# Optimization experiments

Hardware: AMD Instinct MI355X
Metric: run time of the kernel (lower is better)

The kernel has to match this reference:

```python
import jax, jax.numpy as jnp
from jax import lax
import numpy as np

B, S, E, HID = 16, 7, 64, 64
RES = (64, 64); D = RES[0] * RES[1]
XLOW, XHIGH = -0.5, 0.5
RLOW, RHIGH = float(np.sqrt(0.01)), float(np.sqrt(0.05))
PIXEL_MULT = 1.0; N_ITER = 3; TSOFT = 1.0 / float(np.sqrt(E))

def _build_grid():
    ranges = [np.linspace(XLOW, XHIGH, r) for r in RES]
    g = np.stack(np.meshgrid(*ranges, indexing='xy'), axis=-1)
    g = g.reshape(RES[0], RES[1], -1).reshape(1, -1, 2)
    return jnp.asarray(g, dtype=jnp.float32)

ABS_GRID = _build_grid()  # [1, D, 2]

def _ln(x, g, b):
    m = jnp.mean(x, -1, keepdims=True)
    v = jnp.mean(jnp.square(x - m), -1, keepdims=True)
    return (x - m) * lax.rsqrt(v + 1e-5) * g + b

def _forward(data, slot_noise, pos_rand, conv0_w, conv0_b, conv1_w, conv1_b, conv2_w, conv2_b,
             dataN_g, dataN_b, queryN_g, queryN_b, toK_w, toK_b, toV_w, toV_b, dense_w, dense_b,
             mlp1_w, mlp1_b, mlp2_w, mlp2_b, gru_wih, gru_whh, gru_bih, gru_bhh,
             alpha1_w, alpha1_b, alpha2_w, alpha2_b, final1_w, final1_b, final2_w, final2_b,
             slots_mu, slots_logsigma):
    dn = ('NCHW', 'OIHW', 'NCHW')
    def conv(x, w, b):
        return lax.conv_general_dilated(x, w, (1, 1), 'SAME', dimension_numbers=dn) + b[None, :, None, None]
    # CNN encoder: Conv-ReLU x3, 'same' padding, k=5
    x = jax.nn.relu(conv(data, conv0_w, conv0_b))
    x = jax.nn.relu(conv(x, conv1_w, conv1_b))
    x = jax.nn.relu(conv(x, conv2_w, conv2_b))
    enc = x.transpose(0, 2, 3, 1).reshape(B, D, HID)
    enc = _ln(enc, dataN_g, dataN_b)

    queries = slots_mu + jnp.exp(slots_logsigma) * slot_noise  # [B,S,E]
    # init_slots: faithful replication (source indexes the SLOT dim, and swaps rlow/rhigh)
    pos_scale = pos_rand.at[:, :2, :].add(-0.5)
    pos_scale = pos_scale.at[:, -1, :].set((RLOW - RHIGH) * pos_rand[:, -1, :] + RHIGH)

    encK = enc @ toK_w + toK_b  # [B,D,E]
    encV = enc @ toV_w + toV_b

    def init_mlp(y):
        y = _ln(y, queryN_g, queryN_b)
        return jax.nn.relu(y @ mlp1_w + mlp1_b) @ mlp2_w + mlp2_b

    def get_kv(ps):
        # per-slot relative grid: [B,S,D,2]
        rel = (ABS_GRID[:, None] - ps[:, :, None, :2]) / ps[:, :, -1][:, :, None, None]
        eg = PIXEL_MULT * (rel @ dense_w + dense_b)  # [B,S,D,E]
        return init_mlp(encK[:, None] + eg), init_mlp(encV[:, None] + eg)

    def att_wts(q, k):
        logits = jnp.einsum('bse,bsde->bsd', q, k) * TSOFT
        att = jax.nn.softmax(logits, axis=1)  # softmax over slots
        wts = att / jnp.sum(att, -1, keepdims=True) + 1e-8
        return att, wts

    def update_frames(wts):
        new_pos = jnp.einsum('bsd,de->bse', wts, ABS_GRID[0])  # [B,S,2]
        d2 = jnp.sum(jnp.square(ABS_GRID[:, None] - new_pos[:, :, None]), -1)  # [B,S,D]
        new_scale = jnp.sqrt(jnp.einsum('bsd,bsd->bs', wts, d2))
        return jnp.concatenate([new_pos, new_scale[..., None]], -1)

    def gru(xg, h):
        gi = xg @ gru_wih.T + gru_bih
        gh = h @ gru_whh.T + gru_bhh
        ir, iz, inn = jnp.split(gi, 3, -1)
        hr, hz, hn = jnp.split(gh, 3, -1)
        r = jax.nn.sigmoid(ir + hr)
        z = jax.nn.sigmoid(iz + hz)
        n = jnp.tanh(inn + r * hn)
        return (1.0 - z) * n + z * h

    for _ in range(N_ITER):
        keys, vals = get_kv(pos_scale)
        att, wts = att_wts(_ln(queries, queryN_g, queryN_b), keys)
        pos_scale = update_frames(wts)
        upd = jnp.einsum('bsd,bsde->bse', wts, vals)
        queries = gru(upd.reshape(-1, E), queries.reshape(-1, E)).reshape(B, S, E)

    keys, _ = get_kv(pos_scale)
    att, wts = att_wts(_ln(queries, queryN_g, queryN_b), keys)
    nps = update_frames(wts)
    alpha = jax.nn.sigmoid(jax.nn.relu(queries @ alpha1_w + alpha1_b) @ alpha2_w + alpha2_b)
    slot_feat = jax.nn.relu(queries @ final1_w + final1_b) @ final2_w + final2_b + nps
    return queries, att, slot_feat, alpha

def setup_inputs() -> dict:
    ks = jax.random.split(jax.random.key(0), 20)
    f32 = jnp.float32
    def rn(i, shape, s):
        return jax.random.normal(ks[i], shape, f32) * s
    inp = dict(
        data=jax.random.normal(ks[0], (B, 1, RES[0], RES[1]), f32),
        slot_noise=jax.random.normal(ks[1], (B, S, E), f32),
        pos_rand=jax.random.uniform(ks[2], (B, S, 3), dtype=f32),
        conv0_w=rn(3, (HID, 1, 5, 5), 0.2), conv0_b=jnp.zeros(HID, f32),
        conv1_w=rn(4, (HID, HID, 5, 5), 0.025), conv1_b=jnp.zeros(HID, f32),
        conv2_w=rn(5, (HID, HID, 5, 5), 0.025), conv2_b=jnp.zeros(HID, f32),
        dataN_g=jnp.ones(HID, f32), dataN_b=jnp.zeros(HID, f32),
        queryN_g=jnp.ones(E, f32), queryN_b=jnp.zeros(E, f32),
        toK_w=rn(6, (HID, E), 0.125), toK_b=jnp.zeros(E, f32),
        toV_w=rn(7, (HID, E), 0.125), toV_b=jnp.zeros(E, f32),
        dense_w=rn(8, (2, E), 0.7), dense_b=jnp.zeros(E, f32),
        mlp1_w=rn(9, (E, E), 0.125), mlp1_b=jnp.zeros(E, f32),
        mlp2_w=rn(10, (E, E), 0.125), mlp2_b=jnp.zeros(E, f32),
        gru_wih=rn(11, (3 * E, E), 0.125), gru_whh=rn(12, (3 * E, E), 0.125),
        gru_bih=jnp.zeros(3 * E, f32), gru_bhh=jnp.zeros(3 * E, f32),
        alpha1_w=rn(13, (E, 32), 0.125), alpha1_b=jnp.zeros(32, f32),
        alpha2_w=rn(14, (32, 1), 0.18), alpha2_b=jnp.zeros(1, f32),
        final1_w=rn(15, (E, HID), 0.125), final1_b=jnp.zeros(HID, f32),
        final2_w=rn(16, (HID, 3), 0.125), final2_b=jnp.zeros(3, f32),
        slots_mu=rn(17, (1, 1, E), 1.0),
        slots_logsigma=rn(18, (1, 1, E), 0.01),
    )
    return inp

def reference(data, slot_noise, pos_rand, conv0_w, conv0_b, conv1_w, conv1_b, conv2_w, conv2_b,
              dataN_g, dataN_b, queryN_g, queryN_b, toK_w, toK_b, toV_w, toV_b, dense_w, dense_b,
              mlp1_w, mlp1_b, mlp2_w, mlp2_b, gru_wih, gru_whh, gru_bih, gru_bhh,
              alpha1_w, alpha1_b, alpha2_w, alpha2_b, final1_w, final1_b, final2_w, final2_b,
              slots_mu, slots_logsigma):
    return _forward(data, slot_noise, pos_rand, conv0_w, conv0_b, conv1_w, conv1_b, conv2_w, conv2_b,
                    dataN_g, dataN_b, queryN_g, queryN_b, toK_w, toK_b, toV_w, toV_b, dense_w, dense_b,
                    mlp1_w, mlp1_b, mlp2_w, mlp2_b, gru_wih, gru_whh, gru_bih, gru_bhh,
                    alpha1_w, alpha1_b, alpha2_w, alpha2_b, final1_w, final1_b, final2_w, final2_b,
                    slots_mu, slots_logsigma)
```

## Files before the change

### kernel.cpp

```cpp
#include <hip/hip_runtime.h>
#include <cmath>


#define RLOW_F 0.1f
#define RHIGH_F 0.22360679774997896f

typedef __attribute__((ext_vector_type(8))) __bf16 bf16x8;
typedef __attribute__((ext_vector_type(4))) float f32x4;

__device__ __forceinline__ float wsum64(float v){
  #pragma unroll
  for (int off = 32; off > 0; off >>= 1) v += __shfl_xor(v, off, 64);
  return v;
}
__device__ __forceinline__ float rdlane(float v, int l){
  return __int_as_float(__builtin_amdgcn_readlane(__float_as_int(v), l));
}
__device__ __forceinline__ unsigned short bf16bits(float v){
  __bf16 h = (__bf16)v;
  return *reinterpret_cast<unsigned short*>(&h);
}

__global__ void k_prep(const float* __restrict__ noise, const float* __restrict__ prand,
                       const float* __restrict__ mu, const float* __restrict__ logsig,
                       float* __restrict__ queries, float* __restrict__ ps){
  int row = blockIdx.x;
  int e = threadIdx.x;
  int s = row % 7;
  queries[row*64 + e] = mu[e] + expf(logsig[e]) * noise[row*64 + e];
  if (e < 3){
    float pr = prand[row*3 + e];
    float v;
    if (s < 2)      v = pr - 0.5f;
    else if (s == 6) v = (RLOW_F - RHIGH_F)*pr + RHIGH_F;
    else            v = pr;
    ps[row*3 + e] = v;
  }
}

__global__ __launch_bounds__(256) void k_conv0(const float* __restrict__ in,
                        const float* __restrict__ w, const float* __restrict__ bias,
                        unsigned short* __restrict__ out){
  int bi = blockIdx.x; int b = bi >> 6; int y = bi & 63;
  int t = threadIdx.x; int lane = t & 63; int xg = t >> 6;
  __shared__ float s_in[5*68];
  __shared__ float s_w[64*25];
  __shared__ float s_out[64*65];
  for (int i = t; i < 1600; i += 256) s_w[i] = w[i];
  for (int i = t; i < 340; i += 256){
    int r = i / 68, cx = i % 68;
    int yy = y + r - 2, gx = cx - 2;
    float v = 0.f;
    if (yy >= 0 && yy < 64 && gx >= 0 && gx < 64) v = in[(b*64 + yy)*64 + gx];
    s_in[r*68 + cx] = v;
  }
  __syncthreads();
  int o = lane;
  float bv = bias[o];
  float acc[16];
  #pragma unroll
  for (int k = 0; k < 16; k++) acc[k] = bv;
  #pragma unroll
  for (int ky = 0; ky < 5; ky++){
    float rv[20];
    const float4* p = reinterpret_cast<const float4*>(&s_in[ky*68 + xg*16]);
    #pragma unroll
    for (int q = 0; q < 5; q++){ float4 f = p[q]; rv[q*4]=f.x; rv[q*4+1]=f.y; rv[q*4+2]=f.z; rv[q*4+3]=f.w; }
    #pragma unroll
    for (int kx = 0; kx < 5; kx++){
      float wv = s_w[o*25 + ky*5 + kx];
      #pragma unroll
      for (int k = 0; k < 16; k++) acc[k] = fmaf(rv[k+kx], wv, acc[k]);
    }
  }
  #pragma unroll
  for (int k = 0; k < 16; k++) s_out[o*65 + xg*16 + k] = fmaxf(acc[k], 0.f);
  __syncthreads();
  for (int i = t; i < 4096; i += 256){
    int px = i >> 6, ch = i & 63;
    out[((size_t)(b*64 + y)*64 + px)*64 + ch] = bf16bits(s_out[ch*65 + px]);
  }
}

__global__ void k_packconv(const float* __restrict__ w, unsigned short* __restrict__ out){
  int idx = blockIdx.x*256 + threadIdx.x;
  if (idx >= 102400) return;
  int j = idx & 7;
  int l = (idx >> 3) & 63;
  int frag = idx >> 9;
  int nt = frag & 3;
  int ks = (frag >> 2) % 10;
  int dy = frag / 40;
  int q = l >> 4, cr = l & 15;
  int k = ks*32 + q*8 + j;
  int kx = k >> 6, ch = k & 63;
  int n = nt*16 + cr;
  out[idx] = bf16bits(w[((n*64 + ch)*5 + dy)*5 + kx]);
}

__global__ __launch_bounds__(256) void k_convm(const unsigned short* __restrict__ in_bf,
                        const unsigned short* __restrict__ wpack,
                        const float* __restrict__ bias,
                        const float* __restrict__ lng, const float* __restrict__ lnb,
                        unsigned short* __restrict__ out_bf, float* __restrict__ out_f,
                        int mode){
  int bi = blockIdx.x;
  int b = bi >> 4; int yg = bi & 15;
  int t = threadIdx.x; int wv = t >> 6; int l = t & 63;
  int q = l >> 4, cr = l & 15;
  int p0 = wv*16;

  __shared__ char lds[8*68*144];

  for (int ri = 0; ri < 8; ri++){
    int yy = yg*4 + ri - 2;
    bool rok = (yy >= 0 && yy < 64);
    const uint4* src = reinterpret_cast<const uint4*>(in_bf + (size_t)(b*64 + yy)*64*64);
    for (int i = t; i < 544; i += 256){
      int px = i >> 3, c8 = i & 7;
      uint4 v = {0u,0u,0u,0u};
      int gx = px - 2;
      if (rok && gx >= 0 && gx < 64) v = src[gx*8 + c8];
      *reinterpret_cast<uint4*>(&lds[ri*9792 + px*144 + c8*16]) = v;
    }
  }
  __syncthreads();

  f32x4 acc[4][4];
  #pragma unroll
  for (int r = 0; r < 4; r++)
    #pragma unroll
    for (int nt = 0; nt < 4; nt++) acc[r][nt] = (f32x4){0.f,0.f,0.f,0.f};

  const bf16x8* wp = reinterpret_cast<const bf16x8*>(wpack);
  for (int dy = 0; dy < 5; dy++){
    for (int ks = 0; ks < 10; ks++){
      bf16x8 Bf[4];
      int fbase = (dy*10 + ks)*4;
      #pragma unroll
      for (int nt = 0; nt < 4; nt++) Bf[nt] = wp[(fbase + nt)*64 + l];
      int aoff = (p0 + cr + (ks >> 1))*144 + (ks & 1)*64 + q*16;
      #pragma unroll
      for (int r = 0; r < 4; r++){
        bf16x8 a = *reinterpret_cast<const bf16x8*>(&lds[(r + dy)*9792 + aoff]);
        #pragma unroll
        for (int nt = 0; nt < 4; nt++)
          acc[r][nt] = __builtin_amdgcn_mfma_f32_16x16x32_bf16(a, Bf[nt], acc[r][nt], 0, 0, 0);
      }
    }
  }

  float bv[4];
  #pragma unroll
  for (int nt = 0; nt < 4; nt++) bv[nt] = bias[nt*16 + cr];

  if (mode == 0){
    #pragma unroll
    for (int r = 0; r < 4; r++){
      int y = yg*4 + r;
      #pragma unroll
      for (int reg = 0; reg < 4; reg++){
        int p = p0 + q*4 + reg;
        size_t base = ((size_t)(b*64 + y)*64 + p)*64;
        #pragma unroll
        for (int nt = 0; nt < 4; nt++)
          out_bf[base + nt*16 + cr] = bf16bits(fmaxf(acc[r][nt][reg] + bv[nt], 0.f));
      }
    }
  } else {
    float gv[4], bb[4];
    #pragma unroll
    for (int nt = 0; nt < 4; nt++){ gv[nt] = lng[nt*16 + cr]; bb[nt] = lnb[nt*16 + cr]; }
    #pragma unroll
    for (int r = 0; r < 4; r++){
      int y = yg*4 + r;
      #pragma unroll
      for (int reg = 0; reg < 4; reg++){
        int p = p0 + q*4 + reg;
        float v[4]; float s1 = 0.f, s2 = 0.f;
        #pragma unroll
        for (int nt = 0; nt < 4; nt++){
          v[nt] = fmaxf(acc[r][nt][reg] + bv[nt], 0.f);
          s1 += v[nt]; s2 += v[nt]*v[nt];
        }
        #pragma unroll
        for (int m = 1; m < 16; m <<= 1){ s1 += __shfl_xor(s1, m, 64); s2 += __shfl_xor(s2, m, 64); }
        float mean = s1 * (1.f/64.f);
        float var  = s2 * (1.f/64.f) - mean*mean;
        float rstd = 1.0f/sqrtf(var + 1e-5f);
        size_t base = ((size_t)b*4096 + y*64 + p)*64;
        #pragma unroll
        for (int nt = 0; nt < 4; nt++)
          out_f[base + nt*16 + cr] = (v[nt] - mean)*rstd*gv[nt] + bb[nt];
      }
    }
  }
}

__global__ void k_packw1(const float* __restrict__ w1, unsigned short* __restrict__ out){
  int idx = blockIdx.x*256 + threadIdx.x;
  int jj = idx & 7;
  int lane = (idx >> 3) & 63;
  int frag = idx >> 9;
  int ks = frag >> 2, nt = frag & 3;
  int q = lane >> 4, cr = lane & 15;
  int k = ks*32 + q*8 + jj;
  int n = nt*16 + cr;
  out[idx] = bf16bits(w1[k*64 + n]);
}

__global__ __launch_bounds__(256) void k_projm(const float* __restrict__ enc,
                       const unsigned short* __restrict__ kpack, const float* __restrict__ bk,
                       const unsigned short* __restrict__ vpack, const float* __restrict__ bvp,
                       float* __restrict__ K, float* __restrict__ V){
  int bi = blockIdx.x; int b = bi >> 6; int tile = bi & 63;
  int t = threadIdx.x; int wv = t >> 6; int l = t & 63;
  int q = l >> 4, cr = l & 15;
  int d0 = tile*64 + wv*16;

  const bf16x8* kp = reinterpret_cast<const bf16x8*>(kpack);
  const bf16x8* vp = reinterpret_cast<const bf16x8*>(vpack);
  bf16x8 KB[8], VB[8];
  #pragma unroll
  for (int f = 0; f < 8; f++){ KB[f] = kp[f*64 + l]; VB[f] = vp[f*64 + l]; }

  const float* er = enc + (size_t)(b*4096 + d0 + cr)*64;
  bf16x8 a0, a1;
  #pragma unroll
  for (int h = 0; h < 2; h++){
    const float4* e4 = reinterpret_cast<const float4*>(er + (h ? (32 + q*8) : (q*8)));
    #pragma unroll
    for (int p = 0; p < 2; p++){
      float4 e = e4[p];
      if (h == 0){ a0[p*4+0]=(__bf16)e.x; a0[p*4+1]=(__bf16)e.y; a0[p*4+2]=(__bf16)e.z; a0[p*4+3]=(__bf16)e.w; }
      else       { a1[p*4+0]=(__bf16)e.x; a1[p*4+1]=(__bf16)e.y; a1[p*4+2]=(__bf16)e.z; a1[p*4+3]=(__bf16)e.w; }
    }
  }

  f32x4 zero = {0.f,0.f,0.f,0.f};
  f32x4 aK[4], aV[4];
  #pragma unroll
  for (int nt = 0; nt < 4; nt++){
    aK[nt] = __builtin_amdgcn_mfma_f32_16x16x32_bf16(a0, KB[nt],     zero,   0, 0, 0);
    aK[nt] = __builtin_amdgcn_mfma_f32_16x16x32_bf16(a1, KB[4 + nt], aK[nt], 0, 0, 0);
    aV[nt] = __builtin_amdgcn_mfma_f32_16x16x32_bf16(a0, VB[nt],     zero,   0, 0, 0);
    aV[nt] = __builtin_amdgcn_mfma_f32_16x16x32_bf16(a1, VB[4 + nt], aV[nt], 0, 0, 0);
  }
  #pragma unroll
  for (int nt = 0; nt < 4; nt++){
    float bkv = bk[nt*16 + cr], bvv = bvp[nt*16 + cr];
    #pragma unroll
    for (int reg = 0; reg < 4; reg++){
      size_t base = ((size_t)b*4096 + d0 + q*4 + reg)*64 + nt*16 + cr;
      K[base] = aK[nt][reg] + bkv;
      V[base] = aV[nt][reg] + bvv;
    }
  }
}

__global__ void k_phaseprep(const float* __restrict__ queries, const float* __restrict__ ps,
                            const float* __restrict__ qg_, const float* __restrict__ qb_,
                            const float* __restrict__ dw, const float* __restrict__ db,
                            const float* __restrict__ mlp2w, const float* __restrict__ mlp2b,
                            float* __restrict__ absc, float* __restrict__ w2qc,
                            float* __restrict__ sum_att, float* __restrict__ upd){
  int row = blockIdx.x; int e = threadIdx.x;
  float q = queries[row*64 + e];
  float m = wsum64(q) * (1.f/64.f);
  float d = q - m;
  float var = wsum64(d*d) * (1.f/64.f);
  float qlnv = d * (1.0f/sqrtf(var + 1e-5f)) * qg_[e] + qb_[e];
  float px = ps[row*3], py = ps[row*3+1], sc = ps[row*3+2];
  float A  = dw[e]      / sc;
  float Bv = dw[64 + e] / sc;
  absc[(row*3+0)*64 + e] = A;
  absc[(row*3+1)*64 + e] = Bv;
  absc[(row*3+2)*64 + e] = db[e] - px*A - py*Bv;
  float acc = 0.f;
  const float* wrow = mlp2w + e*64;
  for (int j = 0; j < 64; j++) acc = fmaf(wrow[j], rdlane(qlnv, j), acc);
  w2qc[row*68 + e] = acc;
  float c2 = wsum64(mlp2b[e] * qlnv);
  if (e == 0) w2qc[row*68 + 64] = c2;
  upd[row*64 + e] = 0.f;
  if (e == 0) sum_att[row] = 0.f;
}

__global__ __launch_bounds__(256) void k_attn(const float* __restrict__ encX,
     const unsigned short* __restrict__ w1pack, const float* __restrict__ mlp1b,
     const float* __restrict__ absc, const float* __restrict__ qg_,
     const float* __restrict__ qb_, const float* __restrict__ w2qc,
     const float* __restrict__ att, const float* __restrict__ sum_att,
     float* __restrict__ outp, int mode){
  int t = threadIdx.x; int wv = t >> 6; int l = t & 63;
  int q = l >> 4, cr = l & 15;
  int bs = blockIdx.x >> 6; int tile = blockIdx.x & 63;
  int b = bs / 7;
  int m0 = tile*64 + wv*16;
  int drow = m0 + cr;

  const bf16x8* wp = reinterpret_cast<const bf16x8*>(w1pack);
  bf16x8 Bf[8];
  #pragma unroll
  for (int f = 0; f < 8; f++) Bf[f] = wp[f*64 + l];

  const float* Ac = absc + bs*192;
  const float* er = encX + (size_t)(b*4096 + drow)*64;
  float gx = -0.5f + (float)(drow & 63) * (1.f/63.f);
  float gy = -0.5f + (float)((drow >> 6) & 63) * (1.f/63.f);
  float x[16];
  #pragma unroll
  for (int h = 0; h < 2; h++){
    int fb = h ? (32 + q*8) : (q*8);
    const float4* e4 = reinterpret_cast<const float4*>(er + fb);
    const float4* A4 = reinterpret_cast<const float4*>(Ac + fb);
    const float4* B4 = reinterpret_cast<const float4*>(Ac + 64 + fb);
    const float4* C4 = reinterpret_cast<const float4*>(Ac + 128 + fb);
    #pragma unroll
    for (int p = 0; p < 2; p++){
      float4 e = e4[p], Av = A4[p], Bv = B4[p], Cv = C4[p];
      int o = h*8 + p*4;
      x[o+0] = e.x + gx*Av.x + gy*Bv.x + Cv.x;
      x[o+1] = e.y + gx*Av.y + gy*Bv.y + Cv.y;
      x[o+2] = e.z + gx*Av.z + gy*Bv.z + Cv.z;
      x[o+3] = e.w + gx*Av.w + gy*Bv.w + Cv.w;
    }
  }
  float s = 0.f;
  #pragma unroll
  for (int k = 0; k < 16; k++) s += x[k];
  s += __shfl_xor(s, 16, 64); s += __shfl_xor(s, 32, 64);
  float m = s * (1.f/64.f);
  float v = 0.f;
  #pragma unroll
  for (int k = 0; k < 16; k++){ float dd = x[k] - m; v += dd*dd; }
  v += __shfl_xor(v, 16, 64); v += __shfl_xor(v, 32, 64);
  float rstd = 1.0f/sqrtf(v * (1.f/64.f) + 1e-5f);

  bf16x8 a0, a1;
  #pragma unroll
  for (int h = 0; h < 2; h++){
    int fb = h ? (32 + q*8) : (q*8);
    const float4* g4 = reinterpret_cast<const float4*>(qg_ + fb);
    const float4* b4 = reinterpret_cast<const float4*>(qb_ + fb);
    #pragma unroll
    for (int p = 0; p < 2; p++){
      float4 gg = g4[p], bb = b4[p];
      int o = h*8 + p*4;
      float r0 = (x[o+0]-m)*rstd*gg.x + bb.x;
      float r1 = (x[o+1]-m)*rstd*gg.y + bb.y;
      float r2 = (x[o+2]-m)*rstd*gg.z + bb.z;
      float r3 = (x[o+3]-m)*rstd*gg.w + bb.w;
      if (h == 0){ a0[p*4+0]=(__bf16)r0; a0[p*4+1]=(__bf16)r1; a0[p*4+2]=(__bf16)r2; a0[p*4+3]=(__bf16)r3; }
      else       { a1[p*4+0]=(__bf16)r0; a1[p*4+1]=(__bf16)r1; a1[p*4+2]=(__bf16)r2; a1[p*4+3]=(__bf16)r3; }
    }
  }

  f32x4 zero = {0.f, 0.f, 0.f, 0.f};
  f32x4 acc[4];
  #pragma unroll
  for (int nt = 0; nt < 4; nt++){
    acc[nt] = __builtin_amdgcn_mfma_f32_16x16x32_bf16(a0, Bf[nt],     zero,    0, 0, 0);
    acc[nt] = __builtin_amdgcn_mfma_f32_16x16x32_bf16(a1, Bf[4 + nt], acc[nt], 0, 0, 0);
  }

  if (mode == 0){
    const float* wq = w2qc + bs*68;
    float c2 = wq[64];
    float p[4] = {0.f, 0.f, 0.f, 0.f};
    #pragma unroll
    for (int nt = 0; nt < 4; nt++){
      float bb  = mlp1b[nt*16 + cr];
      float wqv = wq[nt*16 + cr];
      #pragma unroll
      for (int reg = 0; reg < 4; reg++){
        float y = fmaxf(acc[nt][reg] + bb, 0.f);
        p[reg] = fmaf(y, wqv, p[reg]);
      }
    }
    #pragma unroll
    for (int reg = 0; reg < 4; reg++){
      #pragma unroll
      for (int off = 1; off < 16; off <<= 1) p[reg] += __shfl_xor(p[reg], off, 64);
    }
    if (cr == 0){
      #pragma unroll
      for (int reg = 0; reg < 4; reg++)
        outp[bs*4096 + m0 + q*4 + reg] = (p[reg] + c2) * 0.125f;
    }
  } else {
    float sa = sum_att[bs];
    float wr[4];
    #pragma unroll
    for (int reg = 0; reg < 4; reg++)
      wr[reg] = att[bs*4096 + m0 + q*4 + reg] / sa + 1e-8f;
    float pc[4] = {0.f, 0.f, 0.f, 0.f};
    #pragma unroll
    for (int nt = 0; nt < 4; nt++){
      float bb = mlp1b[nt*16 + cr];
      #pragma unroll
      for (int reg = 0; reg < 4; reg++)
        pc[nt] = fmaf(wr[reg], fmaxf(acc[nt][reg] + bb, 0.f), pc[nt]);
    }
    #pragma unroll
    for (int nt = 0; nt < 4; nt++){
      pc[nt] += __shfl_xor(pc[nt], 16, 64);
      pc[nt] += __shfl_xor(pc[nt], 32, 64);
    }
    __shared__ float red[4][64];
    if (q == 0){
      #pragma unroll
      for (int nt = 0; nt < 4; nt++) red[wv][nt*16 + cr] = pc[nt];
    }
    __syncthreads();
    if (t < 64) atomicAdd(&outp[bs*64 + t], red[0][t] + red[1][t] + red[2][t] + red[3][t]);
  }
}

__global__ void k_softmax(float* __restrict__ att, float* __restrict__ sum_att){
  int bi = blockIdx.x;
  int b = bi >> 4;
  int t = threadIdx.x;
  int d = (bi & 15)*256 + t;
  int lane = t & 63; int w = t >> 6;
  __shared__ float red[4];
  float l[7];
  #pragma unroll
  for (int s = 0; s < 7; s++) l[s] = att[(b*7+s)*4096 + d];
  float m = l[0];
  #pragma unroll
  for (int s = 1; s < 7; s++) m = fmaxf(m, l[s]);
  float sum = 0.f;
  #pragma unroll
  for (int s = 0; s < 7; s++){ l[s] = expf(l[s] - m); sum += l[s]; }
  for (int s = 0; s < 7; s++){
    float a = l[s] / sum;
    att[(b*7+s)*4096 + d] = a;
    float ws = wsum64(a);
    if (lane == 0) red[w] = ws;
    __syncthreads();
    if (t == 0) atomicAdd(&sum_att[b*7+s], red[0]+red[1]+red[2]+red[3]);
    __syncthreads();
  }
}

__global__ void k_frames(const float* __restrict__ att, const float* __restrict__ sum_att,
                         float* __restrict__ psout, float* __restrict__ sumw){
  int bs = blockIdx.x; int t = threadIdx.x;
  float sa = sum_att[bs];
  float a0 = 0.f, ax = 0.f, ay = 0.f, a2 = 0.f;
  for (int d = t; d < 4096; d += 256){
    float wv = att[bs*4096 + d] / sa + 1e-8f;
    float gx = -0.5f + (float)(d & 63) * (1.f/63.f);
    float gy = -0.5f + (float)(d >> 6) * (1.f/63.f);
    a0 += wv; ax += wv*gx; ay += wv*gy; a2 += wv*(gx*gx + gy*gy);
  }
  __shared__ float red[4][4];
  int lane = t & 63, w = t >> 6;
  a0 = wsum64(a0); ax = wsum64(ax); ay = wsum64(ay); a2 = wsum64(a2);
  if (lane == 0){ red[w][0]=a0; red[w][1]=ax; red[w][2]=ay; red[w][3]=a2; }
  __syncthreads();
  if (t == 0){
    float W0=0,Wx=0,Wy=0,Wg=0;
    for (int k = 0; k < 4; k++){ W0+=red[k][0]; Wx+=red[k][1]; Wy+=red[k][2]; Wg+=red[k][3]; }
    float s2 = Wg - (Wx*Wx + Wy*Wy)*(2.f - W0);
    psout[bs*3+0] = Wx; psout[bs*3+1] = Wy; psout[bs*3+2] = sqrtf(fmaxf(s2, 0.f));
    sumw[bs] = W0;
  }
}

__global__ void k_gru(const float* __restrict__ upd, float* __restrict__ queries,
                      const float* __restrict__ wih, const float* __restrict__ whh,
                      const float* __restrict__ bih, const float* __restrict__ bhh,
                      const float* __restrict__ mlp2w, const float* __restrict__ mlp2b,
                      const float* __restrict__ sumw){
  int row = blockIdx.x; int t = threadIdx.x;
  __shared__ float us[64], hs[64], xs[64], gis[192], ghs[192];
  if (t < 64){ us[t] = upd[row*64 + t]; hs[t] = queries[row*64 + t]; }
  __syncthreads();
  if (t < 64){
    float a = sumw[row] * mlp2b[t];
    for (int i = 0; i < 64; i++) a = fmaf(us[i], mlp2w[i*64 + t], a);
    xs[t] = a;
  }
  __syncthreads();
  float gi = bih[t], gh = bhh[t];
  for (int e = 0; e < 64; e++){
    gi = fmaf(wih[t*64 + e], xs[e], gi);
    gh = fmaf(whh[t*64 + e], hs[e], gh);
  }
  gis[t] = gi; ghs[t] = gh;
  __syncthreads();
  if (t < 64){
    float r = 1.0f/(1.0f + expf(-(gis[t]      + ghs[t])));
    float z = 1.0f/(1.0f + expf(-(gis[64+t]   + ghs[64+t])));
    float n = tanhf(gis[128+t] + r*ghs[128+t]);
    queries[row*64 + t] = (1.0f - z)*n + z*hs[t];
  }
}

__global__ void k_final(const float* __restrict__ queries, const float* __restrict__ nps,
                        const float* __restrict__ a1w, const float* __restrict__ a1b,
                        const float* __restrict__ a2w, const float* __restrict__ a2b,
                        const float* __restrict__ f1w, const float* __restrict__ f1b,
                        const float* __restrict__ f2w, const float* __restrict__ f2b,
                        float* __restrict__ out){
  int bs = blockIdx.x; int e = threadIdx.x;
  __shared__ float qs[64], hf[64], ha[32];
  float q = queries[bs*64 + e];
  qs[e] = q;
  out[bs*64 + e] = q;
  __syncthreads();
  float accf = f1b[e];
  for (int i = 0; i < 64; i++) accf = fmaf(qs[i], f1w[i*64 + e], accf);
  hf[e] = fmaxf(accf, 0.f);
  if (e < 32){
    float acca = a1b[e];
    for (int i = 0; i < 64; i++) acca = fmaf(qs[i], a1w[i*32 + e], acca);
    ha[e] = fmaxf(acca, 0.f);
  }
  __syncthreads();
  if (e < 3){
    float sf = f2b[e];
    for (int o = 0; o < 64; o++) sf = fmaf(hf[o], f2w[o*3 + e], sf);
    out[465920 + bs*3 + e] = sf + nps[bs*3 + e];
  }
  if (e == 32){
    float al = a2b[0];
    for (int o = 0; o < 32; o++) al = fmaf(ha[o], a2w[o], al);
    out[466256 + bs] = 1.0f/(1.0f + expf(-al));
  }
}

extern "C" void kernel_launch(void* const* d_in, const int* in_sizes, int n_in,
                              void* d_out, int out_size, void* d_ws, size_t ws_size,
                              hipStream_t stream){
  const float* data        = (const float*)d_in[0];
  const float* slot_noise  = (const float*)d_in[1];
  const float* pos_rand    = (const float*)d_in[2];
  const float* conv0_w     = (const float*)d_in[3];
  const float* conv0_b     = (const float*)d_in[4];
  const float* conv1_w     = (const float*)d_in[5];
  const float* conv1_b     = (const float*)d_in[6];
  const float* conv2_w     = (const float*)d_in[7];
  const float* conv2_b     = (const float*)d_in[8];
  const float* dataN_g     = (const float*)d_in[9];
  const float* dataN_b     = (const float*)d_in[10];
  const float* queryN_g    = (const float*)d_in[11];
  const float* queryN_b    = (const float*)d_in[12];
  const float* toK_w       = (const float*)d_in[13];
  const float* toK_b       = (const float*)d_in[14];
  const float* toV_w       = (const float*)d_in[15];
  const float* toV_b       = (const float*)d_in[16];
  const float* dense_w     = (const float*)d_in[17];
  const float* dense_b     = (const float*)d_in[18];
  const float* mlp1_w      = (const float*)d_in[19];
  const float* mlp1_b      = (const float*)d_in[20];
  const float* mlp2_w      = (const float*)d_in[21];
  const float* mlp2_b      = (const float*)d_in[22];
  const float* gru_wih     = (const float*)d_in[23];
  const float* gru_whh     = (const float*)d_in[24];
  const float* gru_bih     = (const float*)d_in[25];
  const float* gru_bhh     = (const float*)d_in[26];
  const float* alpha1_w    = (const float*)d_in[27];
  const float* alpha1_b    = (const float*)d_in[28];
  const float* alpha2_w    = (const float*)d_in[29];
  const float* alpha2_b    = (const float*)d_in[30];
  const float* final1_w    = (const float*)d_in[31];
  const float* final1_b    = (const float*)d_in[32];
  const float* final2_w    = (const float*)d_in[33];
  const float* final2_b    = (const float*)d_in[34];
  const float* slots_mu    = (const float*)d_in[35];
  const float* slots_lsig  = (const float*)d_in[36];

  float* ws   = (float*)d_ws;
  float* bufA = ws;
  float* bufB = bufA + 4194304;
  float* bufC = bufB + 4194304;
  float* attw = bufC + 4194304;
  float* queries = attw + 458752;
  float* ps   = queries + 7168;
  float* absc = ps + 512;
  float* sum_att = absc + 21504;
  float* upd  = sum_att + 128;
  float* nps  = upd + 7168;
  float* w2qc = nps + 512;
  float* sumw = w2qc + 7616;
  unsigned short* w1pack = (unsigned short*)(sumw + 128);
  unsigned short* kpack  = w1pack + 4096;
  unsigned short* vpack  = kpack + 4096;
  unsigned short* wp1    = vpack + 4096;
  unsigned short* wp2    = wp1 + 102400;

  unsigned short* c0_bf = (unsigned short*)bufA;
  unsigned short* c1_bf = (unsigned short*)bufC;
  float* enc  = bufB;
  float* encK = bufA;
  float* encV = bufC;

  float* outq   = (float*)d_out;
  float* outatt = outq + 7168;

  k_prep<<<112, 64, 0, stream>>>(slot_noise, pos_rand, slots_mu, slots_lsig, queries, ps);
  k_packw1<<<16, 256, 0, stream>>>(mlp1_w, w1pack);
  k_packw1<<<16, 256, 0, stream>>>(toK_w, kpack);
  k_packw1<<<16, 256, 0, stream>>>(toV_w, vpack);
  k_packconv<<<400, 256, 0, stream>>>(conv1_w, wp1);
  k_packconv<<<400, 256, 0, stream>>>(conv2_w, wp2);
  k_conv0<<<1024, 256, 0, stream>>>(data, conv0_w, conv0_b, c0_bf);
  k_convm<<<256, 256, 0, stream>>>(c0_bf, wp1, conv1_b, nullptr, nullptr, c1_bf, nullptr, 0);
  k_convm<<<256, 256, 0, stream>>>(c1_bf, wp2, conv2_b, dataN_g, dataN_b, nullptr, enc, 1);
  k_projm<<<1024, 256, 0, stream>>>(enc, kpack, toK_b, vpack, toV_b, encK, encV);

  for (int p = 0; p < 4; p++){
    float* attp = (p == 3) ? outatt : attw;
    k_phaseprep<<<112, 64, 0, stream>>>(queries, ps, queryN_g, queryN_b, dense_w, dense_b,
                                        mlp2_w, mlp2_b, absc, w2qc, sum_att, upd);
    k_attn<<<7168, 256, 0, stream>>>(encK, w1pack, mlp1_b, absc, queryN_g, queryN_b,
                                     w2qc, attp, sum_att, attp, 0);
    k_softmax<<<256, 256, 0, stream>>>(attp, sum_att);
    k_frames<<<112, 256, 0, stream>>>(attp, sum_att, (p == 3) ? nps : ps, sumw);
    if (p < 3){
      k_attn<<<7168, 256, 0, stream>>>(encV, w1pack, mlp1_b, absc, queryN_g, queryN_b,
                                       w2qc, attp, sum_att, upd, 1);
      k_gru<<<112, 192, 0, stream>>>(upd, queries, gru_wih, gru_whh, gru_bih, gru_bhh,
                                     mlp2_w, mlp2_b, sumw);
    }
  }
  k_final<<<112, 64, 0, stream>>>(queries, nps, alpha1_w, alpha1_b, alpha2_w, alpha2_b,
                                  final1_w, final1_b, final2_w, final2_b, outq);
}
```

Measured before the change: 595.7 us.

## Fuse slot loop and softmax into attention kernels, fold phaseprep into prep/GRU

The attention kernels now give each block one batch's 64-pixel tile and loop over all 7 slots inside it. Encoder rows and LayerNorm params are loaded once and reused across slots, and per-slot coefficients are staged in shared memory. The slot softmax and the sum_att reduction move into the K-attention kernel, so the separate softmax launch and the logits round trip through global memory go away. The V kernel accumulates updates in shared memory before issuing global atomics, and the per-phase prep work is folded into k_prep and k_gru, which removes one launch per iteration. In exchange there are 1024 blocks instead of 7168, each doing serial slot iterations, which lowers parallelism.

```diff
diff --git a/kernel.cpp b/kernel.cpp
--- a/kernel.cpp
+++ b/kernel.cpp
@@ -21,21 +21,55 @@
   return *reinterpret_cast<unsigned short*>(&h);
 }
 
+__device__ __forceinline__ void pp_core(int row, int e, float qv,
+    float px, float py, float sc,
+    const float* __restrict__ qg_, const float* __restrict__ qb_,
+    const float* __restrict__ dw, const float* __restrict__ db,
+    const float* __restrict__ mlp2w, const float* __restrict__ mlp2b,
+    float* __restrict__ absc, float* __restrict__ w2qc,
+    float* __restrict__ sum_att){
+  float m = wsum64(qv) * (1.f/64.f);
+  float d = qv - m;
+  float var = wsum64(d*d) * (1.f/64.f);
+  float qlnv = d * (1.0f/sqrtf(var + 1e-5f)) * qg_[e] + qb_[e];
+  float A  = dw[e]      / sc;
+  float Bv = dw[64 + e] / sc;
+  absc[row*192 + e]       = A;
+  absc[row*192 + 64 + e]  = Bv;
+  absc[row*192 + 128 + e] = db[e] - px*A - py*Bv;
+  float acc = 0.f;
+  const float* wrow = mlp2w + e*64;
+  for (int j = 0; j < 64; j++) acc = fmaf(wrow[j], rdlane(qlnv, j), acc);
+  w2qc[row*68 + e] = acc;
+  float c2 = wsum64(mlp2b[e] * qlnv);
+  if (e == 0){ w2qc[row*68 + 64] = c2; sum_att[row] = 0.f; }
+}
+
 __global__ void k_prep(const float* __restrict__ noise, const float* __restrict__ prand,
                        const float* __restrict__ mu, const float* __restrict__ logsig,
-                       float* __restrict__ queries, float* __restrict__ ps){
+                       const float* __restrict__ qg_, const float* __restrict__ qb_,
+                       const float* __restrict__ dw, const float* __restrict__ db,
+                       const float* __restrict__ mlp2w, const float* __restrict__ mlp2b,
+                       float* __restrict__ queries, float* __restrict__ ps,
+                       float* __restrict__ absc, float* __restrict__ w2qc,
+                       float* __restrict__ sum_att, float* __restrict__ upd){
   int row = blockIdx.x;
   int e = threadIdx.x;
   int s = row % 7;
-  queries[row*64 + e] = mu[e] + expf(logsig[e]) * noise[row*64 + e];
+  float qv = mu[e] + expf(logsig[e]) * noise[row*64 + e];
+  queries[row*64 + e] = qv;
+  upd[row*64 + e] = 0.f;
+  float pv = 0.f;
   if (e < 3){
     float pr = prand[row*3 + e];
-    float v;
-    if (s < 2)      v = pr - 0.5f;
-    else if (s == 6) v = (RLOW_F - RHIGH_F)*pr + RHIGH_F;
-    else            v = pr;
-    ps[row*3 + e] = v;
-  }
+    if (s < 2)       pv = pr - 0.5f;
+    else if (s == 6) pv = (RLOW_F - RHIGH_F)*pr + RHIGH_F;
+    else             pv = pr;
+    ps[row*3 + e] = pv;
+  }
+  float px = rdlane(pv, 0), py = rdlane(pv, 1), sc = rdlane(pv, 2);
+  pp_core(row, e, qv, px, py, sc, qg_, qb_, dw, db, mlp2w, mlp2b,
+          absc, w2qc, sum_att);
 }
 
 __global__ __launch_bounds__(256) void k_conv0(const float* __restrict__ in,
@@ -258,190 +292,264 @@
   }
 }
 
-__global__ void k_phaseprep(const float* __restrict__ queries, const float* __restrict__ ps,
-                            const float* __restrict__ qg_, const float* __restrict__ qb_,
-                            const float* __restrict__ dw, const float* __restrict__ db,
-                            const float* __restrict__ mlp2w, const float* __restrict__ mlp2b,
-                            float* __restrict__ absc, float* __restrict__ w2qc,
-                            float* __restrict__ sum_att, float* __restrict__ upd){
-  int row = blockIdx.x; int e = threadIdx.x;
-  float q = queries[row*64 + e];
-  float m = wsum64(q) * (1.f/64.f);
-  float d = q - m;
-  float var = wsum64(d*d) * (1.f/64.f);
-  float qlnv = d * (1.0f/sqrtf(var + 1e-5f)) * qg_[e] + qb_[e];
-  float px = ps[row*3], py = ps[row*3+1], sc = ps[row*3+2];
-  float A  = dw[e]      / sc;
-  float Bv = dw[64 + e] / sc;
-  absc[(row*3+0)*64 + e] = A;
-  absc[(row*3+1)*64 + e] = Bv;
-  absc[(row*3+2)*64 + e] = db[e] - px*A - py*Bv;
-  float acc = 0.f;
-  const float* wrow = mlp2w + e*64;
-  for (int j = 0; j < 64; j++) acc = fmaf(wrow[j], rdlane(qlnv, j), acc);
-  w2qc[row*68 + e] = acc;
-  float c2 = wsum64(mlp2b[e] * qlnv);
-  if (e == 0) w2qc[row*68 + 64] = c2;
-  upd[row*64 + e] = 0.f;
-  if (e == 0) sum_att[row] = 0.f;
-}
-
-__global__ __launch_bounds__(256) void k_attn(const float* __restrict__ encX,
+__global__ __launch_bounds__(256) void k_attnK(const float* __restrict__ encX,
      const unsigned short* __restrict__ w1pack, const float* __restrict__ mlp1b,
      const float* __restrict__ absc, const float* __restrict__ qg_,
      const float* __restrict__ qb_, const float* __restrict__ w2qc,
-     const float* __restrict__ att, const float* __restrict__ sum_att,
-     float* __restrict__ outp, int mode){
+     float* __restrict__ att, float* __restrict__ sum_att){
+  int bi = blockIdx.x;
+  int b = bi >> 6, tile = bi & 63;
   int t = threadIdx.x; int wv = t >> 6; int l = t & 63;
   int q = l >> 4, cr = l & 15;
-  int bs = blockIdx.x >> 6; int tile = blockIdx.x & 63;
-  int b = bs / 7;
   int m0 = tile*64 + wv*16;
   int drow = m0 + cr;
 
+  __shared__ float s_log[7*64];
+  __shared__ float s_absc[7*192];
+  __shared__ float s_wq[7*68];
+  for (int i = t; i < 1344; i += 256) s_absc[i] = absc[b*7*192 + i];
+  for (int i = t; i < 476;  i += 256) s_wq[i]   = w2qc[b*7*68 + i];
+
   const bf16x8* wp = reinterpret_cast<const bf16x8*>(w1pack);
   bf16x8 Bf[8];
   #pragma unroll
   for (int f = 0; f < 8; f++) Bf[f] = wp[f*64 + l];
 
-  const float* Ac = absc + bs*192;
   const float* er = encX + (size_t)(b*4096 + drow)*64;
   float gx = -0.5f + (float)(drow & 63) * (1.f/63.f);
   float gy = -0.5f + (float)((drow >> 6) & 63) * (1.f/63.f);
-  float x[16];
+  float xb[16], gq[16], bq[16];
   #pragma unroll
   for (int h = 0; h < 2; h++){
     int fb = h ? (32 + q*8) : (q*8);
     const float4* e4 = reinterpret_cast<const float4*>(er + fb);
-    const float4* A4 = reinterpret_cast<const float4*>(Ac + fb);
-    const float4* B4 = reinterpret_cast<const float4*>(Ac + 64 + fb);
-    const float4* C4 = reinterpret_cast<const float4*>(Ac + 128 + fb);
+    const float4* g4 = reinterpret_cast<const float4*>(qg_ + fb);
+    const float4* b4 = reinterpret_cast<const float4*>(qb_ + fb);
     #pragma unroll
     for (int p = 0; p < 2; p++){
-      float4 e = e4[p], Av = A4[p], Bv = B4[p], Cv = C4[p];
+      float4 e = e4[p], gg = g4[p], bb = b4[p];
       int o = h*8 + p*4;
-      x[o+0] = e.x + gx*Av.x + gy*Bv.x + Cv.x;
-      x[o+1] = e.y + gx*Av.y + gy*Bv.y + Cv.y;
-      x[o+2] = e.z + gx*Av.z + gy*Bv.z + Cv.z;
-      x[o+3] = e.w + gx*Av.w + gy*Bv.w + Cv.w;
-    }
-  }
-  float s = 0.f;
-  #pragma unroll
-  for (int k = 0; k < 16; k++) s += x[k];
-  s += __shfl_xor(s, 16, 64); s += __shfl_xor(s, 32, 64);
-  float m = s * (1.f/64.f);
-  float v = 0.f;
-  #pragma unroll
-  for (int k = 0; k < 16; k++){ float dd = x[k] - m; v += dd*dd; }
-  v += __shfl_xor(v, 16, 64); v += __shfl_xor(v, 32, 64);
-  float rstd = 1.0f/sqrtf(v * (1.f/64.f) + 1e-5f);
-
-  bf16x8 a0, a1;
+      xb[o+0]=e.x; xb[o+1]=e.y; xb[o+2]=e.z; xb[o+3]=e.w;
+      gq[o+0]=gg.x; gq[o+1]=gg.y; gq[o+2]=gg.z; gq[o+3]=gg.w;
+      bq[o+0]=bb.x; bq[o+1]=bb.y; bq[o+2]=bb.z; bq[o+3]=bb.w;
+    }
+  }
+  float b1v[4];
+  #pragma unroll
+  for (int nt = 0; nt < 4; nt++) b1v[nt] = mlp1b[nt*16 + cr];
+  __syncthreads();
+
+  for (int s = 0; s < 7; s++){
+    const float* Ac = s_absc + s*192;
+    float x[16];
+    #pragma unroll
+    for (int h = 0; h < 2; h++){
+      int fb = h ? (32 + q*8) : (q*8);
+      const float4* A4 = reinterpret_cast<const float4*>(Ac + fb);
+      const float4* B4 = reinterpret_cast<const float4*>(Ac + 64 + fb);
+      const float4* C4 = reinterpret_cast<const float4*>(Ac + 128 + fb);
+      #pragma unroll
+      for (int p = 0; p < 2; p++){
+        float4 Av = A4[p], Bv = B4[p], Cv = C4[p];
+        int o = h*8 + p*4;
+        x[o+0] = xb[o+0] + gx*Av.x + gy*Bv.x + Cv.x;
+        x[o+1] = xb[o+1] + gx*Av.y + gy*Bv.y + Cv.y;
+        x[o+2] = xb[o+2] + gx*Av.z + gy*Bv.z + Cv.z;
+        x[o+3] = xb[o+3] + gx*Av.w + gy*Bv.w + Cv.w;
+      }
+    }
+    float sum = 0.f;
+    #pragma unroll
+    for (int k = 0; k < 16; k++) sum += x[k];
+    sum += __shfl_xor(sum, 16, 64); sum += __shfl_xor(sum, 32, 64);
+    float m = sum * (1.f/64.f);
+    float v = 0.f;
+    #pragma unroll
+    for (int k = 0; k < 16; k++){ float dd = x[k] - m; v += dd*dd; }
+    v += __shfl_xor(v, 16, 64); v += __shfl_xor(v, 32, 64);
+    float rstd = 1.0f/sqrtf(v * (1.f/64.f) + 1e-5f);
+
+    bf16x8 a0, a1;
+    #pragma unroll
+    for (int k = 0; k < 8; k++)  a0[k] = (__bf16)((x[k]   - m)*rstd*gq[k]   + bq[k]);
+    #pragma unroll
+    for (int k = 0; k < 8; k++)  a1[k] = (__bf16)((x[8+k] - m)*rstd*gq[8+k] + bq[8+k]);
+
+    f32x4 zero = {0.f, 0.f, 0.f, 0.f};
+    f32x4 acc[4];
+    #pragma unroll
+    for (int nt = 0; nt < 4; nt++){
+      acc[nt] = __builtin_amdgcn_mfma_f32_16x16x32_bf16(a0, Bf[nt],     zero,    0, 0, 0);
+      acc[nt] = __builtin_amdgcn_mfma_f32_16x16x32_bf16(a1, Bf[4 + nt], acc[nt], 0, 0, 0);
+    }
+
+    float c2 = s_wq[s*68 + 64];
+    float p[4] = {0.f, 0.f, 0.f, 0.f};
+    #pragma unroll
+    for (int nt = 0; nt < 4; nt++){
+      float wqv = s_wq[s*68 + nt*16 + cr];
+      #pragma unroll
+      for (int reg = 0; reg < 4; reg++){
+        float y = fmaxf(acc[nt][reg] + b1v[nt], 0.f);
+        p[reg] = fmaf(y, wqv, p[reg]);
+      }
+    }
+    #pragma unroll
+    for (int reg = 0; reg < 4; reg++){
+      #pragma unroll
+      for (int off = 1; off < 16; off <<= 1) p[reg] += __shfl_xor(p[reg], off, 64);
+    }
+    if (cr == 0){
+      #pragma unroll
+      for (int reg = 0; reg < 4; reg++)
+        s_log[s*64 + wv*16 + q*4 + reg] = (p[reg] + c2) * 0.125f;
+    }
+  }
+  __syncthreads();
+
+  if (t < 64){
+    float lv[7];
+    #pragma unroll
+    for (int s = 0; s < 7; s++) lv[s] = s_log[s*64 + t];
+    float mx = lv[0];
+    #pragma unroll
+    for (int s = 1; s < 7; s++) mx = fmaxf(mx, lv[s]);
+    float sm = 0.f;
+    #pragma unroll
+    for (int s = 0; s < 7; s++){ lv[s] = expf(lv[s] - mx); sm += lv[s]; }
+    float inv = 1.0f / sm;
+    for (int s = 0; s < 7; s++){
+      float a = lv[s] * inv;
+      att[(size_t)(b*7+s)*4096 + tile*64 + t] = a;
+      float ws = wsum64(a);
+      if (t == 0) atomicAdd(&sum_att[b*7+s], ws);
+    }
+  }
+}
+
+__global__ __launch_bounds__(256) void k_attnV(const float* __restrict__ encX,
+     const unsigned short* __restrict__ w1pack, const float* __restrict__ mlp1b,
+     const float* __restrict__ absc, const float* __restrict__ qg_,
+     const float* __restrict__ qb_, const float* __restrict__ att,
+     const float* __restrict__ sum_att, float* __restrict__ upd){
+  int bi = blockIdx.x;
+  int b = bi >> 6, tile = bi & 63;
+  int t = threadIdx.x; int wv = t >> 6; int l = t & 63;
+  int q = l >> 4, cr = l & 15;
+  int m0 = tile*64 + wv*16;
+  int drow = m0 + cr;
+
+  __shared__ float s_absc[7*192];
+  __shared__ float s_att[7*64];
+  __shared__ float s_upd[7*64];
+  __shared__ float s_inv[7];
+  for (int i = t; i < 1344; i += 256) s_absc[i] = absc[b*7*192 + i];
+  for (int i = t; i < 448;  i += 256){
+    s_att[i] = att[(size_t)(b*7 + (i >> 6))*4096 + tile*64 + (i & 63)];
+    s_upd[i] = 0.f;
+  }
+  if (t < 7) s_inv[t] = 1.0f / sum_att[b*7 + t];
+
+  const bf16x8* wp = reinterpret_cast<const bf16x8*>(w1pack);
+  bf16x8 Bf[8];
+  #pragma unroll
+  for (int f = 0; f < 8; f++) Bf[f] = wp[f*64 + l];
+
+  const float* er = encX + (size_t)(b*4096 + drow)*64;
+  float gx = -0.5f + (float)(drow & 63) * (1.f/63.f);
+  float gy = -0.5f + (float)((drow >> 6) & 63) * (1.f/63.f);
+  float xb[16], gq[16], bq[16];
   #pragma unroll
   for (int h = 0; h < 2; h++){
     int fb = h ? (32 + q*8) : (q*8);
+    const float4* e4 = reinterpret_cast<const float4*>(er + fb);
     const float4* g4 = reinterpret_cast<const float4*>(qg_ + fb);
     const float4* b4 = reinterpret_cast<const float4*>(qb_ + fb);
     #pragma unroll
     for (int p = 0; p < 2; p++){
-      float4 gg = g4[p], bb = b4[p];
+      float4 e = e4[p], gg = g4[p], bb = b4[p];
       int o = h*8 + p*4;
-      float r0 = (x[o+0]-m)*rstd*gg.x + bb.x;
-      float r1 = (x[o+1]-m)*rstd*gg.y + bb.y;
-      float r2 = (x[o+2]-m)*rstd*gg.z + bb.z;
-      float r3 = (x[o+3]-m)*rstd*gg.w + bb.w;
-      if (h == 0){ a0[p*4+0]=(__bf16)r0; a0[p*4+1]=(__bf16)r1; a0[p*4+2]=(__bf16)r2; a0[p*4+3]=(__bf16)r3; }
-      else       { a1[p*4+0]=(__bf16)r0; a1[p*4+1]=(__bf16)r1; a1[p*4+2]=(__bf16)r2; a1[p*4+3]=(__bf16)r3; }
-    }
-  }
-
-  f32x4 zero = {0.f, 0.f, 0.f, 0.f};
-  f32x4 acc[4];
-  #pragma unroll
-  for (int nt = 0; nt < 4; nt++){
-    acc[nt] = __builtin_amdgcn_mfma_f32_16x16x32_bf16(a0, Bf[nt],     zero,    0, 0, 0);
-    acc[nt] = __builtin_amdgcn_mfma_f32_16x16x32_bf16(a1, Bf[4 + nt], acc[nt], 0, 0, 0);
-  }
-
-  if (mode == 0){
-    const float* wq = w2qc + bs*68;
-    float c2 = wq[64];
-    float p[4] = {0.f, 0.f, 0.f, 0.f};
+      xb[o+0]=e.x; xb[o+1]=e.y; xb[o+2]=e.z; xb[o+3]=e.w;
+      gq[o+0]=gg.x; gq[o+1]=gg.y; gq[o+2]=gg.z; gq[o+3]=gg.w;
+      bq[o+0]=bb.x; bq[o+1]=bb.y; bq[o+2]=bb.z; bq[o+3]=bb.w;
+    }
+  }
+  float b1v[4];
+  #pragma unroll
+  for (int nt = 0; nt < 4; nt++) b1v[nt] = mlp1b[nt*16 + cr];
+  __syncthreads();
+
+  for (int s = 0; s < 7; s++){
+    const float* Ac = s_absc + s*192;
+    float x[16];
+    #pragma unroll
+    for (int h = 0; h < 2; h++){
+      int fb = h ? (32 + q*8) : (q*8);
+      const float4* A4 = reinterpret_cast<const float4*>(Ac + fb);
+      const float4* B4 = reinterpret_cast<const float4*>(Ac + 64 + fb);
+      const float4* C4 = reinterpret_cast<const float4*>(Ac + 128 + fb);
+      #pragma unroll
+      for (int p = 0; p < 2; p++){
+        float4 Av = A4[p], Bv = B4[p], Cv = C4[p];
+        int o = h*8 + p*4;
+        x[o+0] = xb[o+0] + gx*Av.x + gy*Bv.x + Cv.x;
+        x[o+1] = xb[o+1] + gx*Av.y + gy*Bv.y + Cv.y;
+        x[o+2] = xb[o+2] + gx*Av.z + gy*Bv.z + Cv.z;
+        x[o+3] = xb[o+3] + gx*Av.w + gy*Bv.w + Cv.w;
+      }
+    }
+    float sum = 0.f;
+    #pragma unroll
+    for (int k = 0; k < 16; k++) sum += x[k];
+    sum += __shfl_xor(sum, 16, 64); sum += __shfl_xor(sum, 32, 64);
+    float m = sum * (1.f/64.f);
+    float v = 0.f;
+    #pragma unroll
+    for (int k = 0; k < 16; k++){ float dd = x[k] - m; v += dd*dd; }
+    v += __shfl_xor(v, 16, 64); v += __shfl_xor(v, 32, 64);
+    float rstd = 1.0f/sqrtf(v * (1.f/64.f) + 1e-5f);
+
+    bf16x8 a0, a1;
+    #pragma unroll
+    for (int k = 0; k < 8; k++)  a0[k] = (__bf16)((x[k]   - m)*rstd*gq[k]   + bq[k]);
+    #pragma unroll
+    for (int k = 0; k < 8; k++)  a1[k] = (__bf16)((x[8+k] - m)*rstd*gq[8+k] + bq[8+k]);
+
+    f32x4 zero = {0.f, 0.f, 0.f, 0.f};
+    f32x4 acc[4];
     #pragma unroll
     for (int nt = 0; nt < 4; nt++){
-      float bb  = mlp1b[nt*16 + cr];
-      float wqv = wq[nt*16 + cr];
-      #pragma unroll
-      for (int reg = 0; reg < 4; reg++){
-        float y = fmaxf(acc[nt][reg] + bb, 0.f);
-        p[reg] = fmaf(y, wqv, p[reg]);
-      }
-    }
-    #pragma unroll
-    for (int reg = 0; reg < 4; reg++){
-      #pragma unroll
-      for (int off = 1; off < 16; off <<= 1) p[reg] += __shfl_xor(p[reg], off, 64);
-    }
-    if (cr == 0){
+      acc[nt] = __builtin_amdgcn_mfma_f32_16x16x32_bf16(a0, Bf[nt],     zero,    0, 0, 0);
+      acc[nt] = __builtin_amdgcn_mfma_f32_16x16x32_bf16(a1, Bf[4 + nt], acc[nt], 0, 0, 0);
+    }
+
+    float rsa = s_inv[s];
+    float wr[4];
+    #pragma unroll
+    for (int reg = 0; reg < 4; reg++)
+      wr[reg] = fmaf(s_att[s*64 + wv*16 + q*4 + reg], rsa, 1e-8f);
+    float pc[4];
+    #pragma unroll
+    for (int nt = 0; nt < 4; nt++){
+      pc[nt] = 0.f;
       #pragma unroll
       for (int reg = 0; reg < 4; reg++)
-        outp[bs*4096 + m0 + q*4 + reg] = (p[reg] + c2) * 0.125f;
-    }
-  } else {
-    float sa = sum_att[bs];
-    float wr[4];
-    #pragma unroll
-    for (int reg = 0; reg < 4; reg++)
-      wr[reg] = att[bs*4096 + m0 + q*4 + reg] / sa + 1e-8f;
-    float pc[4] = {0.f, 0.f, 0.f, 0.f};
-    #pragma unroll
-    for (int nt = 0; nt < 4; nt++){
-      float bb = mlp1b[nt*16 + cr];
-      #pragma unroll
-      for (int reg = 0; reg < 4; reg++)
-        pc[nt] = fmaf(wr[reg], fmaxf(acc[nt][reg] + bb, 0.f), pc[nt]);
+        pc[nt] = fmaf(wr[reg], fmaxf(acc[nt][reg] + b1v[nt], 0.f), pc[nt]);
     }
     #pragma unroll
     for (int nt = 0; nt < 4; nt++){
       pc[nt] += __shfl_xor(pc[nt], 16, 64);
       pc[nt] += __shfl_xor(pc[nt], 32, 64);
     }
-    __shared__ float red[4][64];
     if (q == 0){
       #pragma unroll
-      for (int nt = 0; nt < 4; nt++) red[wv][nt*16 + cr] = pc[nt];
-    }
-    __syncthreads();
-    if (t < 64) atomicAdd(&outp[bs*64 + t], red[0][t] + red[1][t] + red[2][t] + red[3][t]);
-  }
-}
-
-__global__ void k_softmax(float* __restrict__ att, float* __restrict__ sum_att){
-  int bi = blockIdx.x;
-  int b = bi >> 4;
-  int t = threadIdx.x;
-  int d = (bi & 15)*256 + t;
-  int lane = t & 63; int w = t >> 6;
-  __shared__ float red[4];
-  float l[7];
-  #pragma unroll
-  for (int s = 0; s < 7; s++) l[s] = att[(b*7+s)*4096 + d];
-  float m = l[0];
-  #pragma unroll
-  for (int s = 1; s < 7; s++) m = fmaxf(m, l[s]);
-  float sum = 0.f;
-  #pragma unroll
-  for (int s = 0; s < 7; s++){ l[s] = expf(l[s] - m); sum += l[s]; }
-  for (int s = 0; s < 7; s++){
-    float a = l[s] / sum;
-    att[(b*7+s)*4096 + d] = a;
-    float ws = wsum64(a);
-    if (lane == 0) red[w] = ws;
-    __syncthreads();
-    if (t == 0) atomicAdd(&sum_att[b*7+s], red[0]+red[1]+red[2]+red[3]);
-    __syncthreads();
-  }
+      for (int nt = 0; nt < 4; nt++)
+        atomicAdd(&s_upd[s*64 + nt*16 + cr], pc[nt]);
+    }
+  }
+  __syncthreads();
+  for (int i = t; i < 448; i += 256)
+    atomicAdd(&upd[b*448 + i], s_upd[i]);
 }
 
 __global__ void k_frames(const float* __restrict__ att, const float* __restrict__ sum_att,
@@ -469,11 +577,15 @@
   }
 }
 
-__global__ void k_gru(const float* __restrict__ upd, float* __restrict__ queries,
+__global__ void k_gru(float* __restrict__ upd, float* __restrict__ queries,
                       const float* __restrict__ wih, const float* __restrict__ whh,
                       const float* __restrict__ bih, const float* __restrict__ bhh,
                       const float* __restrict__ mlp2w, const float* __restrict__ mlp2b,
-                      const float* __restrict__ sumw){
+                      const float* __restrict__ sumw, const float* __restrict__ ps,
+                      const float* __restrict__ qg_, const float* __restrict__ qb_,
+                      const float* __restrict__ dw, const float* __restrict__ db,
+                      float* __restrict__ absc, float* __restrict__ w2qc,
+                      float* __restrict__ sum_att){
   int row = blockIdx.x; int t = threadIdx.x;
   __shared__ float us[64], hs[64], xs[64], gis[192], ghs[192];
   if (t < 64){ us[t] = upd[row*64 + t]; hs[t] = queries[row*64 + t]; }
@@ -495,7 +607,12 @@
     float r = 1.0f/(1.0f + expf(-(gis[t]      + ghs[t])));
     float z = 1.0f/(1.0f + expf(-(gis[64+t]   + ghs[64+t])));
     float n = tanhf(gis[128+t] + r*ghs[128+t]);
-    queries[row*64 + t] = (1.0f - z)*n + z*hs[t];
+    float newq = (1.0f - z)*n + z*hs[t];
+    queries[row*64 + t] = newq;
+    upd[row*64 + t] = 0.f;
+    float px = ps[row*3], py = ps[row*3+1], sc = ps[row*3+2];
+    pp_core(row, t, newq, px, py, sc, qg_, qb_, dw, db, mlp2w, mlp2b,
+            absc, w2qc, sum_att);
   }
 }
 
@@ -601,7 +718,9 @@
   float* outq   = (float*)d_out;
   float* outatt = outq + 7168;
 
-  k_prep<<<112, 64, 0, stream>>>(slot_noise, pos_rand, slots_mu, slots_lsig, queries, ps);
+  k_prep<<<112, 64, 0, stream>>>(slot_noise, pos_rand, slots_mu, slots_lsig,
+                                 queryN_g, queryN_b, dense_w, dense_b, mlp2_w, mlp2_b,
+                                 queries, ps, absc, w2qc, sum_att, upd);
   k_packw1<<<16, 256, 0, stream>>>(mlp1_w, w1pack);
   k_packw1<<<16, 256, 0, stream>>>(toK_w, kpack);
   k_packw1<<<16, 256, 0, stream>>>(toV_w, vpack);
@@ -614,17 +733,15 @@
 
   for (int p = 0; p < 4; p++){
     float* attp = (p == 3) ? outatt : attw;
-    k_phaseprep<<<112, 64, 0, stream>>>(queries, ps, queryN_g, queryN_b, dense_w, dense_b,
-                                        mlp2_w, mlp2_b, absc, w2qc, sum_att, upd);
-    k_attn<<<7168, 256, 0, stream>>>(encK, w1pack, mlp1_b, absc, queryN_g, queryN_b,
-                                     w2qc, attp, sum_att, attp, 0);
-    k_softmax<<<256, 256, 0, stream>>>(attp, sum_att);
+    k_attnK<<<1024, 256, 0, stream>>>(encK, w1pack, mlp1_b, absc, queryN_g, queryN_b,
+                                      w2qc, attp, sum_att);
     k_frames<<<112, 256, 0, stream>>>(attp, sum_att, (p == 3) ? nps : ps, sumw);
     if (p < 3){
-      k_attn<<<7168, 256, 0, stream>>>(encV, w1pack, mlp1_b, absc, queryN_g, queryN_b,
-                                       w2qc, attp, sum_att, upd, 1);
+      k_attnV<<<1024, 256, 0, stream>>>(encV, w1pack, mlp1_b, absc, queryN_g, queryN_b,
+                                        attp, sum_att, upd);
       k_gru<<<112, 192, 0, stream>>>(upd, queries, gru_wih, gru_whh, gru_bih, gru_bhh,
-                                     mlp2_w, mlp2_b, sumw);
+                                     mlp2_w, mlp2_b, sumw, ps, queryN_g, queryN_b,
+                                     dense_w, dense_b, absc, w2qc, sum_att);
     }
   }
   k_final<<<112, 64, 0, stream>>>(queries, nps, alpha1_w, alpha1_b, alpha2_w, alpha2_b,
```

Measured after the change: 565.7 us. 5.0% less time.
